# Performance work log

Hardware: AMD Instinct MI355X
Metric: run time of the kernel (lower is better)

## Reference

```python
import jax, jax.numpy as jnp
import numpy as np

NA = 3
ANCHORS = np.array([1.28967, 4.15014, 2.12714, 5.09344, 3.27212, 5.87423], dtype=np.float32)
OBJECT_SCALE = 5.0
NOOBJECT_SCALE = 1.0
CLASS_SCALE = 1.0
COORD_SCALE = 1.0
SIL_THRESH = 0.6
GAMMA = 0.5
EPS = 1e-7


def _iou_cxcywh(b1, b2):
    # b1, b2: [..., 4] as (cx, cy, w, h); broadcasting elementwise IoU
    mx = jnp.minimum(b1[..., 0] - b1[..., 2] * 0.5, b2[..., 0] - b2[..., 2] * 0.5)
    Mx = jnp.maximum(b1[..., 0] + b1[..., 2] * 0.5, b2[..., 0] + b2[..., 2] * 0.5)
    my = jnp.minimum(b1[..., 1] - b1[..., 3] * 0.5, b2[..., 1] - b2[..., 3] * 0.5)
    My = jnp.maximum(b1[..., 1] + b1[..., 3] * 0.5, b2[..., 1] + b2[..., 3] * 0.5)
    uw = Mx - mx
    uh = My - my
    cw = b1[..., 2] + b2[..., 2] - uw
    ch = b1[..., 3] + b2[..., 3] - uh
    inter = jnp.where((cw <= 0) | (ch <= 0), 0.0, cw * ch)
    union = b1[..., 2] * b1[..., 3] + b2[..., 2] * b2[..., 3] - inter
    return inter / union


def setup_inputs() -> dict:
    key = jax.random.key(0)
    k1, k2, k3, k4, k5 = jax.random.split(key, 5)
    nB, nC, nH, nW = 32, 80, 56, 56
    output = jax.random.normal(k1, (nB, NA * (5 + nC), nH, nW), dtype=jnp.float32)
    cxy = jax.random.uniform(k2, (nB, 50, 2), minval=0.02, maxval=0.98)
    wh = jax.random.uniform(k3, (nB, 50, 2), minval=0.05, maxval=0.6)
    target_boxes = jnp.concatenate([cxy, wh], axis=-1).astype(jnp.float32)
    target_cls = (jax.random.uniform(k4, (nB, 50, nC)) < 0.05).astype(jnp.float32)
    class_weight = jax.random.uniform(k5, (nC,), dtype=jnp.float32)
    return {"output": output, "target_boxes": target_boxes,
            "target_cls": target_cls, "class_weight": class_weight}


def reference(output, target_boxes, target_cls, class_weight):
    sg = jax.lax.stop_gradient
    anchors = jnp.asarray(ANCHORS)
    aw_all, ah_all = anchors[0::2], anchors[1::2]          # [nA]
    nB, _, nH, nW = output.shape
    nC = class_weight.shape[0]
    nA = NA
    out = output.reshape(nB, nA, 5 + nC, nH, nW)
    x = jax.nn.sigmoid(out[:, :, 0])                        # [nB,nA,nH,nW]
    y = jax.nn.sigmoid(out[:, :, 1])
    w = out[:, :, 2]
    h = out[:, :, 3]
    conf = jax.nn.sigmoid(out[:, :, 4])
    # class probs: [nB,nA,nH,nW,nC] (matches torch view/transpose to [nB*nA*nH*nW, nC])
    p_cls = jax.nn.sigmoid(jnp.transpose(out[:, :, 5:], (0, 1, 3, 4, 2)))

    grid_x = jnp.arange(nW, dtype=jnp.float32)[None, None, None, :]
    grid_y = jnp.arange(nH, dtype=jnp.float32)[None, None, :, None]
    # predicted boxes in grid units (detached, as torch uses .data)
    px = sg(x) + grid_x
    py = sg(y) + grid_y
    pw = jnp.exp(sg(w)) * aw_all[None, :, None, None]
    ph = jnp.exp(sg(h)) * ah_all[None, :, None, None]
    pred = jnp.stack([px, py, pw, ph], axis=-1).reshape(nB, nA * nH * nW, 4)

    # ---- build_targets (vectorized over (b, t, anchor*cell)) ----
    scale = jnp.array([nW, nH, nW, nH], dtype=jnp.float32)
    g = sg(target_boxes) * scale                            # [nB,50,4] grid units
    valid = target_boxes[:, :, 2] > 0                       # [nB,50]
    # IoU of every gt against every predicted box; max over gt -> silence mask
    ious = _iou_cxcywh(g[:, :, None, :], pred[:, None, :, :])  # [nB,50,nA*nH*nW]
    max_iou = jnp.max(jnp.where(valid[:, :, None], ious, 0.0), axis=1)
    conf_mask = jnp.where(max_iou > SIL_THRESH, 0.0, NOOBJECT_SCALE)  # [nB,nA*nH*nW]

    gx, gy, gw, gh = g[..., 0], g[..., 1], g[..., 2], g[..., 3]
    # best anchor by centered-box IoU: inter = min(w)*min(h)
    inter_a = jnp.minimum(aw_all, gw[..., None]) * jnp.minimum(ah_all, gh[..., None])
    union_a = aw_all * ah_all + (gw * gh)[..., None] - inter_a
    best_n = jnp.argmax(inter_a / union_a, axis=-1)         # [nB,50]

    gi = jnp.clip(gx.astype(jnp.int32), 0, nW - 1)
    gj = jnp.clip(gy.astype(jnp.int32), 0, nH - 1)
    b_idx = jnp.arange(nB)[:, None]
    flat = ((b_idx * nA + best_n) * nH + gj) * nW + gi      # [nB,50]
    total = nB * nA * nH * nW
    idx = jnp.where(valid, flat, total).reshape(-1)         # invalid -> out-of-range, dropped

    zeros = jnp.zeros((total,), dtype=jnp.float32)
    coord_mask = zeros.at[idx].set(1.0, mode="drop")
    conf_mask = conf_mask.reshape(-1).at[idx].set(OBJECT_SCALE, mode="drop")
    aw_b = aw_all[best_n]
    ah_b = ah_all[best_n]
    tx = zeros.at[idx].set((gx - gi.astype(jnp.float32)).reshape(-1), mode="drop")
    ty = zeros.at[idx].set((gy - gj.astype(jnp.float32)).reshape(-1), mode="drop")
    tw = zeros.at[idx].set(jnp.log(gw / aw_b).reshape(-1), mode="drop")
    th = zeros.at[idx].set(jnp.log(gh / ah_b).reshape(-1), mode="drop")
    pred_flat = pred.reshape(total, 4)
    pred_at = pred_flat[jnp.where(valid, flat, 0).reshape(-1)]  # [nB*50,4]
    iou_gt = _iou_cxcywh(g.reshape(-1, 4), pred_at)
    tconf = zeros.at[idx].set(iou_gt, mode="drop")
    tcls = jnp.zeros((total, nC), dtype=jnp.float32).at[idx].set(
        sg(target_cls).reshape(-1, nC), mode="drop")

    shp = (nB, nA, nH, nW)
    coord_mask = sg(coord_mask.reshape(shp))
    conf_mask = sg(conf_mask.reshape(shp))
    tx, ty, tw, th, tconf = (sg(t.reshape(shp)) for t in (tx, ty, tw, th, tconf))
    tcls = sg(tcls.reshape(nB, nA, nH, nW, nC))

    # ---- losses ----
    loss_x = 0.5 * COORD_SCALE * jnp.sum(coord_mask * (x - tx) ** 2)
    loss_y = 0.5 * COORD_SCALE * jnp.sum(coord_mask * (y - ty) ** 2)
    loss_w = 0.5 * COORD_SCALE * jnp.sum(coord_mask * (w - tw) ** 2)
    loss_h = 0.5 * COORD_SCALE * jnp.sum(coord_mask * (h - th) ** 2)
    # conf_mask is sqrt'ed then squared inside MSE -> equals conf_mask weighting
    loss_conf = 0.5 * jnp.sum(conf_mask * (conf - tconf) ** 2)

    # binary focal loss over cells selected by cls_mask (== coord_mask), size-averaged
    l1 = (1.0 - p_cls + EPS) ** GAMMA * jnp.log(p_cls + EPS) * jnp.exp(class_weight)
    l0 = (p_cls + EPS) ** GAMMA * jnp.log(1.0 - p_cls + EPS) * jnp.exp(1.0 - class_weight)
    per_el = tcls * l1 + (1.0 - tcls) * l0
    nsel = jnp.maximum(jnp.sum(coord_mask), 1.0)
    loss_cls = CLASS_SCALE * (-jnp.sum(coord_mask[..., None] * per_el) / nsel)

    return loss_x + loss_y + loss_w + loss_h + loss_conf + loss_cls
```

## Files before the change

kernel.cpp:

```cpp
#include <hip/hip_runtime.h>
#include <math.h>

#define NB 32
#define NA 3
#define NC 80
#define NH 56
#define NW 56
#define NT 50
#define HW (NH*NW)
#define CELLS_PER_B (NA*HW)
#define CH_PER_A (5+NC)
#define EPSF 1e-7f
#define NBLK_X ((CELLS_PER_B + 255) / 256)
#define NBLK (NBLK_X * NB)

__device__ __forceinline__ float fsig(float v) { return 1.0f / (1.0f + __expf(-v)); }

__global__ __launch_bounds__(256) void fused_kernel(const float* __restrict__ out,
                                                    const float* __restrict__ tb,
                                                    const float* __restrict__ tcls,
                                                    const float* __restrict__ cwt,
                                                    float4* __restrict__ part) {
    __shared__ float4 sp1[NT], sp2[NT];
    __shared__ int s_obj[NT];
    __shared__ int s_cnt;
    __shared__ float redm[4], redc[4];

    const int b = blockIdx.y;
    const int tid = threadIdx.x;

    const float aw[3] = {1.28967f, 2.12714f, 3.27212f};
    const float ah[3] = {4.15014f, 5.09344f, 5.87423f};
    const float law[3] = {0.25438842f, 0.75477730f, 1.18543813f};
    const float lah[3] = {1.42314173f, 1.62795138f, 1.77057764f};

    if (tid == 0) s_cnt = 0;
    if (tid < NT) {
        float4 box = ((const float4*)tb)[b * NT + tid];
        float gx = box.x * (float)NW;
        float gy = box.y * (float)NH;
        float gw = box.z * (float)NW;
        float gh = box.w * (float)NH;
        if (box.z > 0.0f) {
            sp1[tid] = make_float4(gx - 0.5f * gw, gx + 0.5f * gw,
                                   gy - 0.5f * gh, gy + 0.5f * gh);
            int bn = 0;
            float best = -1.0f;
            #pragma unroll
            for (int k = 0; k < 3; ++k) {
                float inter = fminf(aw[k], gw) * fminf(ah[k], gh);
                float uni = aw[k] * ah[k] + gw * gh - inter;
                float r = inter / uni;
                if (r > best) { best = r; bn = k; }
            }
            int gi = (int)gx; gi = gi < 0 ? 0 : (gi > NW - 1 ? NW - 1 : gi);
            int gj = (int)gy; gj = gj < 0 ? 0 : (gj > NH - 1 ? NH - 1 : gj);
            int flat_local = (bn * NH + gj) * NW + gi;
            sp2[tid] = make_float4(gw, gh, 0.6f * gw * gh, __int_as_float(flat_local));
        } else {
            sp1[tid] = make_float4(1e9f, 1e9f, 1e9f, 1e9f);
            sp2[tid] = make_float4(0.0f, 0.0f, 0.0f, __int_as_float(-1));
        }
    }
    __syncthreads();

    const int lc = blockIdx.x * blockDim.x + tid;
    float lmain = 0.0f;

    if (lc < CELLS_PER_B) {
        const int a = lc / HW;
        const int rem = lc - a * HW;
        const int j = rem / NW;
        const int i = rem - j * NW;

        const float* base = out + (size_t)b * (NA * CH_PER_A * HW) + (size_t)(a * CH_PER_A) * HW + rem;
        float o0 = base[0];
        float o1 = base[HW];
        float o2 = base[2 * HW];
        float o3 = base[3 * HW];
        float o4 = base[4 * HW];

        float x = fsig(o0);
        float y = fsig(o1);
        float conf = fsig(o4);
        float pw = __expf(o2) * aw[a];
        float ph = __expf(o3) * ah[a];
        float px = x + (float)i;
        float py = y + (float)j;
        float px1 = px - 0.5f * pw, px2 = px + 0.5f * pw;
        float py1 = py - 0.5f * ph, py2 = py + 0.5f * ph;
        float parea06 = 0.6f * (pw * ph);

        bool sil = false;
        int tsel = -1;
        #pragma unroll 5
        for (int t = 0; t < NT; ++t) {
            float4 p1 = sp1[t];
            float4 p2 = sp2[t];
            float mx = fminf(p1.x, px1);
            float Mx = fmaxf(p1.y, px2);
            float my = fminf(p1.z, py1);
            float My = fmaxf(p1.w, py2);
            float cw = (p2.x + pw) - (Mx - mx);
            float ch = (p2.y + ph) - (My - my);
            float inter = fmaxf(cw, 0.0f) * fmaxf(ch, 0.0f);
            sil = sil || (1.6f * inter > (p2.z + parea06));
            if (__float_as_int(p2.w) == lc) tsel = t;
        }

        if (tsel >= 0) {
            float4 g1 = sp1[tsel];
            float4 g2 = sp2[tsel];
            float gx = 0.5f * (g1.x + g1.y);
            float gy = 0.5f * (g1.z + g1.w);
            float tx = gx - (float)i;
            float ty = gy - (float)j;
            float tw = __logf(g2.x) - law[a];
            float th = __logf(g2.y) - lah[a];
            lmain += 0.5f * ((x - tx) * (x - tx) + (y - ty) * (y - ty) +
                             (o2 - tw) * (o2 - tw) + (o3 - th) * (o3 - th));
            float mx = fminf(g1.x, px1), Mx = fmaxf(g1.y, px2);
            float my = fminf(g1.z, py1), My = fmaxf(g1.w, py2);
            float cw = (g2.x + pw) - (Mx - mx);
            float ch = (g2.y + ph) - (My - my);
            float inter = fmaxf(cw, 0.0f) * fmaxf(ch, 0.0f);
            float uni = g2.x * g2.y + (pw * ph) - inter;
            float tconf = inter / uni;
            lmain += 2.5f * (conf - tconf) * (conf - tconf);

            int pos = atomicAdd(&s_cnt, 1);
            s_obj[pos] = (lc << 6) | tsel;
        } else {
            lmain += sil ? 0.0f : 0.5f * conf * conf;
        }
    }
    __syncthreads();

    const int cnt = s_cnt;
    float lcls = 0.0f;
    if (cnt > 0) {
        const int oo = tid / NC;
        const int c = tid - oo * NC;
        if (oo < 3) {
            float w = cwt[c];
            float ew1 = __expf(w);
            float ew0 = __expf(1.0f - w);
            for (int o0 = 0; o0 < cnt; o0 += 3) {
                int o = o0 + oo;
                if (o < cnt) {
                    int pk = s_obj[o];
                    int olc = pk >> 6;
                    int tsel = pk & 63;
                    int a = olc / HW;
                    int rem = olc - a * HW;
                    float p = fsig(out[(size_t)b * (NA * CH_PER_A * HW) +
                                       (size_t)(a * CH_PER_A + 5 + c) * HW + rem]);
                    float t = tcls[(size_t)(b * NT + tsel) * NC + c];
                    float l1 = sqrtf(1.0f - p + EPSF) * __logf(p + EPSF) * ew1;
                    float l0 = sqrtf(p + EPSF) * __logf(1.0f - p + EPSF) * ew0;
                    lcls += t * l1 + (1.0f - t) * l0;
                }
            }
        }
    }

    for (int off = 32; off > 0; off >>= 1) {
        lmain += __shfl_down(lmain, off, 64);
        lcls  += __shfl_down(lcls, off, 64);
    }
    if ((tid & 63) == 0) { redm[tid >> 6] = lmain; redc[tid >> 6] = lcls; }
    __syncthreads();
    if (tid == 0) {
        float m = redm[0] + redm[1] + redm[2] + redm[3];
        float c = redc[0] + redc[1] + redc[2] + redc[3];
        part[blockIdx.y * gridDim.x + blockIdx.x] =
            make_float4(m, c, (float)cnt, 0.0f);
    }
}

__global__ __launch_bounds__(256) void finalize_kernel(const float4* __restrict__ part,
                                                       float* __restrict__ outp) {
    const int tid = threadIdx.x;
    float m = 0.0f, c = 0.0f, n = 0.0f;
    for (int i = tid; i < NBLK; i += 256) {
        float4 p = part[i];
        m += p.x; c += p.y; n += p.z;
    }
    for (int off = 32; off > 0; off >>= 1) {
        m += __shfl_down(m, off, 64);
        c += __shfl_down(c, off, 64);
        n += __shfl_down(n, off, 64);
    }
    __shared__ float rm[4], rc[4], rn[4];
    if ((tid & 63) == 0) { rm[tid >> 6] = m; rc[tid >> 6] = c; rn[tid >> 6] = n; }
    __syncthreads();
    if (tid == 0) {
        float ms = rm[0] + rm[1] + rm[2] + rm[3];
        float cs = rc[0] + rc[1] + rc[2] + rc[3];
        float ns = rn[0] + rn[1] + rn[2] + rn[3];
        float nsel = fmaxf(ns, 1.0f);
        outp[0] = ms - cs / nsel;
    }
}

extern "C" void kernel_launch(void* const* d_in, const int* in_sizes, int n_in,
                              void* d_out, int out_size, void* d_ws, size_t ws_size,
                              hipStream_t stream) {
    const float* output = (const float*)d_in[0];
    const float* tb     = (const float*)d_in[1];
    const float* tcls   = (const float*)d_in[2];
    const float* cwt    = (const float*)d_in[3];

    float4* part = (float4*)d_ws;

    fused_kernel<<<dim3(NBLK_X, NB), 256, 0, stream>>>(output, tb, tcls, cwt, part);
    finalize_kernel<<<1, 256, 0, stream>>>(part, (float*)d_out);
}
```

Measured before the change: 20.95 us.

## Process two cells per thread, use shared cell-to-target map, simplify IoU test

Each thread now handles two cells, which halves the block count to 19 per batch and lets each target-box shared-memory load serve two IoU tests. The per-iteration target-match comparison is replaced by a byte map of all cells in shared memory, filled once by thread 0. The silence test is rewritten as a direct intersection-width check against precomputed 0.375-scaled areas. The trade-offs are a 9.4KB shared map that every block must zero, a serial fill loop on one thread, more registers per thread, and fewer blocks for latency hiding.

```diff
diff --git a/kernel.cpp b/kernel.cpp
--- a/kernel.cpp
+++ b/kernel.cpp
@@ -11,8 +11,10 @@
 #define CELLS_PER_B (NA*HW)
 #define CH_PER_A (5+NC)
 #define EPSF 1e-7f
-#define NBLK_X ((CELLS_PER_B + 255) / 256)
-#define NBLK (NBLK_X * NB)
+#define NBX 19
+#define HALF (NBX*256)
+#define NBLK (NBX*NB)
+#define MAPW (CELLS_PER_B/4)
 
 __device__ __forceinline__ float fsig(float v) { return 1.0f / (1.0f + __expf(-v)); }
 
@@ -21,31 +23,41 @@
                                                     const float* __restrict__ tcls,
                                                     const float* __restrict__ cwt,
                                                     float4* __restrict__ part) {
-    __shared__ float4 sp1[NT], sp2[NT];
-    __shared__ int s_obj[NT];
-    __shared__ int s_cnt;
-    __shared__ float redm[4], redc[4];
+    __shared__ float4 sp1[NT];
+    __shared__ float  sq[NT];
+    __shared__ int    s_flat[NT];
+    __shared__ unsigned char s_map[CELLS_PER_B];
+    __shared__ int    s_obj[NT];
+    __shared__ int    s_cnt;
+    __shared__ float  redm[4], redc[4];
 
     const int b = blockIdx.y;
     const int tid = threadIdx.x;
 
-    const float aw[3] = {1.28967f, 2.12714f, 3.27212f};
-    const float ah[3] = {4.15014f, 5.09344f, 5.87423f};
+    const float aw[3]  = {1.28967f, 2.12714f, 3.27212f};
+    const float ah[3]  = {4.15014f, 5.09344f, 5.87423f};
     const float law[3] = {0.25438842f, 0.75477730f, 1.18543813f};
     const float lah[3] = {1.42314173f, 1.62795138f, 1.77057764f};
 
+    unsigned int* mw = (unsigned int*)s_map;
+    #pragma unroll
+    for (int k = 0; k < 10; ++k) {
+        int idx = tid + k * 256;
+        if (idx < MAPW) mw[idx] = 0u;
+    }
     if (tid == 0) s_cnt = 0;
+
     if (tid < NT) {
         float4 box = ((const float4*)tb)[b * NT + tid];
-        float gx = box.x * (float)NW;
-        float gy = box.y * (float)NH;
-        float gw = box.z * (float)NW;
-        float gh = box.w * (float)NH;
         if (box.z > 0.0f) {
+            float gx = box.x * (float)NW;
+            float gy = box.y * (float)NH;
+            float gw = box.z * (float)NW;
+            float gh = box.w * (float)NH;
             sp1[tid] = make_float4(gx - 0.5f * gw, gx + 0.5f * gw,
                                    gy - 0.5f * gh, gy + 0.5f * gh);
-            int bn = 0;
-            float best = -1.0f;
+            sq[tid] = 0.375f * gw * gh;
+            int bn = 0; float best = -1.0f;
             #pragma unroll
             for (int k = 0; k < 3; ++k) {
                 float inter = fminf(aw[k], gw) * fminf(ah[k], gh);
@@ -55,83 +67,123 @@
             }
             int gi = (int)gx; gi = gi < 0 ? 0 : (gi > NW - 1 ? NW - 1 : gi);
             int gj = (int)gy; gj = gj < 0 ? 0 : (gj > NH - 1 ? NH - 1 : gj);
-            int flat_local = (bn * NH + gj) * NW + gi;
-            sp2[tid] = make_float4(gw, gh, 0.6f * gw * gh, __int_as_float(flat_local));
+            s_flat[tid] = (bn * NH + gj) * NW + gi;
         } else {
-            sp1[tid] = make_float4(1e9f, 1e9f, 1e9f, 1e9f);
-            sp2[tid] = make_float4(0.0f, 0.0f, 0.0f, __int_as_float(-1));
-        }
-    }
-    __syncthreads();
-
-    const int lc = blockIdx.x * blockDim.x + tid;
+            sp1[tid] = make_float4(1e9f, -1e9f, 1e9f, -1e9f);
+            sq[tid] = 0.0f;
+            s_flat[tid] = -1;
+        }
+    }
+    __syncthreads();
+    if (tid == 0) {
+        #pragma unroll
+        for (int t = 0; t < NT; ++t) {
+            int f = s_flat[t];
+            if (f >= 0) s_map[f] = (unsigned char)(t + 1);
+        }
+    }
+    __syncthreads();
+
+    const int c0 = blockIdx.x * 256 + tid;
+    const int c1 = c0 + HALF;
+    const bool v1 = (c1 < CELLS_PER_B);
+
+    const int a0 = c0 / HW;
+    const int rem0 = c0 - a0 * HW;
+    const int j0 = rem0 / NW;
+    const int i0 = rem0 - j0 * NW;
+    const float* base0 = out + (size_t)b * (NA * CH_PER_A * HW) + (size_t)(a0 * CH_PER_A) * HW + rem0;
+    float o00 = base0[0];
+    float o01 = base0[HW];
+    float o02 = base0[2 * HW];
+    float o03 = base0[3 * HW];
+    float o04 = base0[4 * HW];
+
+    const int a1 = v1 ? (c1 / HW) : 0;
+    const int rem1 = c1 - a1 * HW;
+    const int j1 = rem1 / NW;
+    const int i1 = rem1 - j1 * NW;
+    float o10 = 0.f, o11 = 0.f, o12 = 0.f, o13 = 0.f, o14 = 0.f;
+    const float* base1 = out + (size_t)b * (NA * CH_PER_A * HW) + (size_t)(a1 * CH_PER_A) * HW + rem1;
+    if (v1) {
+        o10 = base1[0];
+        o11 = base1[HW];
+        o12 = base1[2 * HW];
+        o13 = base1[3 * HW];
+        o14 = base1[4 * HW];
+    }
+
+    float x0 = fsig(o00), y0 = fsig(o01), conf0 = fsig(o04);
+    float pw0 = __expf(o02) * aw[a0], ph0 = __expf(o03) * ah[a0];
+    float px0 = x0 + (float)i0, py0 = y0 + (float)j0;
+    float px1_0 = px0 - 0.5f * pw0, px2_0 = px0 + 0.5f * pw0;
+    float py1_0 = py0 - 0.5f * ph0, py2_0 = py0 + 0.5f * ph0;
+    float qp0 = 0.375f * pw0 * ph0;
+
+    float x1 = fsig(o10), y1 = fsig(o11), conf1 = fsig(o14);
+    float pw1 = __expf(o12) * aw[a1], ph1 = __expf(o13) * ah[a1];
+    float px1c = x1 + (float)i1, py1c = y1 + (float)j1;
+    float px1_1 = px1c - 0.5f * pw1, px2_1 = px1c + 0.5f * pw1;
+    float py1_1 = py1c - 0.5f * ph1, py2_1 = py1c + 0.5f * ph1;
+    float qp1 = 0.375f * pw1 * ph1;
+
+    bool sil0 = false, sil1 = false;
+    #pragma unroll 5
+    for (int t = 0; t < NT; ++t) {
+        float4 p1 = sp1[t];
+        float qt = sq[t];
+        float iw0 = fminf(p1.y, px2_0) - fmaxf(p1.x, px1_0);
+        float ih0 = fminf(p1.w, py2_0) - fmaxf(p1.z, py1_0);
+        float in0 = fmaxf(iw0, 0.f) * fmaxf(ih0, 0.f);
+        sil0 = sil0 || (in0 > qt + qp0);
+        float iw1 = fminf(p1.y, px2_1) - fmaxf(p1.x, px1_1);
+        float ih1 = fminf(p1.w, py2_1) - fmaxf(p1.z, py1_1);
+        float in1 = fmaxf(iw1, 0.f) * fmaxf(ih1, 0.f);
+        sil1 = sil1 || (in1 > qt + qp1);
+    }
+
+    auto objloss = [&](int tsel, float x, float y, float o2, float o3, float conf,
+                       float px1, float px2, float py1, float py2, float pw, float ph,
+                       int i, int j, int a) -> float {
+        float4 g1 = sp1[tsel];
+        float gw = g1.y - g1.x, gh = g1.w - g1.z;
+        float gx = 0.5f * (g1.x + g1.y), gy = 0.5f * (g1.z + g1.w);
+        float tx = gx - (float)i, ty = gy - (float)j;
+        float tw = __logf(gw) - law[a], th = __logf(gh) - lah[a];
+        float l = 0.5f * ((x - tx) * (x - tx) + (y - ty) * (y - ty) +
+                          (o2 - tw) * (o2 - tw) + (o3 - th) * (o3 - th));
+        float iw = fminf(g1.y, px2) - fmaxf(g1.x, px1);
+        float ih = fminf(g1.w, py2) - fmaxf(g1.z, py1);
+        float inter = fmaxf(iw, 0.f) * fmaxf(ih, 0.f);
+        float uni = gw * gh + pw * ph - inter;
+        float tconf = inter / uni;
+        l += 2.5f * (conf - tconf) * (conf - tconf);
+        return l;
+    };
+
     float lmain = 0.0f;
-
-    if (lc < CELLS_PER_B) {
-        const int a = lc / HW;
-        const int rem = lc - a * HW;
-        const int j = rem / NW;
-        const int i = rem - j * NW;
-
-        const float* base = out + (size_t)b * (NA * CH_PER_A * HW) + (size_t)(a * CH_PER_A) * HW + rem;
-        float o0 = base[0];
-        float o1 = base[HW];
-        float o2 = base[2 * HW];
-        float o3 = base[3 * HW];
-        float o4 = base[4 * HW];
-
-        float x = fsig(o0);
-        float y = fsig(o1);
-        float conf = fsig(o4);
-        float pw = __expf(o2) * aw[a];
-        float ph = __expf(o3) * ah[a];
-        float px = x + (float)i;
-        float py = y + (float)j;
-        float px1 = px - 0.5f * pw, px2 = px + 0.5f * pw;
-        float py1 = py - 0.5f * ph, py2 = py + 0.5f * ph;
-        float parea06 = 0.6f * (pw * ph);
-
-        bool sil = false;
-        int tsel = -1;
-        #pragma unroll 5
-        for (int t = 0; t < NT; ++t) {
-            float4 p1 = sp1[t];
-            float4 p2 = sp2[t];
-            float mx = fminf(p1.x, px1);
-            float Mx = fmaxf(p1.y, px2);
-            float my = fminf(p1.z, py1);
-            float My = fmaxf(p1.w, py2);
-            float cw = (p2.x + pw) - (Mx - mx);
-            float ch = (p2.y + ph) - (My - my);
-            float inter = fmaxf(cw, 0.0f) * fmaxf(ch, 0.0f);
-            sil = sil || (1.6f * inter > (p2.z + parea06));
-            if (__float_as_int(p2.w) == lc) tsel = t;
-        }
-
-        if (tsel >= 0) {
-            float4 g1 = sp1[tsel];
-            float4 g2 = sp2[tsel];
-            float gx = 0.5f * (g1.x + g1.y);
-            float gy = 0.5f * (g1.z + g1.w);
-            float tx = gx - (float)i;
-            float ty = gy - (float)j;
-            float tw = __logf(g2.x) - law[a];
-            float th = __logf(g2.y) - lah[a];
-            lmain += 0.5f * ((x - tx) * (x - tx) + (y - ty) * (y - ty) +
-                             (o2 - tw) * (o2 - tw) + (o3 - th) * (o3 - th));
-            float mx = fminf(g1.x, px1), Mx = fmaxf(g1.y, px2);
-            float my = fminf(g1.z, py1), My = fmaxf(g1.w, py2);
-            float cw = (g2.x + pw) - (Mx - mx);
-            float ch = (g2.y + ph) - (My - my);
-            float inter = fmaxf(cw, 0.0f) * fmaxf(ch, 0.0f);
-            float uni = g2.x * g2.y + (pw * ph) - inter;
-            float tconf = inter / uni;
-            lmain += 2.5f * (conf - tconf) * (conf - tconf);
-
+    {
+        int m0 = (int)s_map[c0];
+        if (m0 > 0) {
+            int tsel = m0 - 1;
+            lmain += objloss(tsel, x0, y0, o02, o03, conf0,
+                             px1_0, px2_0, py1_0, py2_0, pw0, ph0, i0, j0, a0);
             int pos = atomicAdd(&s_cnt, 1);
-            s_obj[pos] = (lc << 6) | tsel;
+            s_obj[pos] = (c0 << 6) | tsel;
         } else {
-            lmain += sil ? 0.0f : 0.5f * conf * conf;
+            lmain += sil0 ? 0.0f : 0.5f * conf0 * conf0;
+        }
+    }
+    if (v1) {
+        int m1 = (int)s_map[c1];
+        if (m1 > 0) {
+            int tsel = m1 - 1;
+            lmain += objloss(tsel, x1, y1, o12, o13, conf1,
+                             px1_1, px2_1, py1_1, py2_1, pw1, ph1, i1, j1, a1);
+            int pos = atomicAdd(&s_cnt, 1);
+            s_obj[pos] = (c1 << 6) | tsel;
+        } else {
+            lmain += sil1 ? 0.0f : 0.5f * conf1 * conf1;
         }
     }
     __syncthreads();
@@ -173,8 +225,7 @@
     if (tid == 0) {
         float m = redm[0] + redm[1] + redm[2] + redm[3];
         float c = redc[0] + redc[1] + redc[2] + redc[3];
-        part[blockIdx.y * gridDim.x + blockIdx.x] =
-            make_float4(m, c, (float)cnt, 0.0f);
+        part[blockIdx.y * NBX + blockIdx.x] = make_float4(m, c, (float)cnt, 0.0f);
     }
 }
 
@@ -213,6 +264,6 @@
 
     float4* part = (float4*)d_ws;
 
-    fused_kernel<<<dim3(NBLK_X, NB), 256, 0, stream>>>(output, tb, tcls, cwt, part);
+    fused_kernel<<<dim3(NBX, NB), 256, 0, stream>>>(output, tb, tcls, cwt, part);
     finalize_kernel<<<1, 256, 0, stream>>>(part, (float*)d_out);
 }
```

Result: slower. 22.21 us (+6.0%).
